# Optimization experiments

Measured on AMD Instinct MI355X. Metric: run time of the kernel, lower is better.

The kernel has to match this reference:

```python
import jax, jax.numpy as jnp
import numpy as np

B, S, DIM, H = 8, 1024, 768, 12
HD = DIM // H  # head_dim = 64
SCALE = HD ** -0.5


def setup_inputs() -> dict:
    key = jax.random.key(0)
    ks = jax.random.split(key, 9)
    std = DIM ** -0.5
    x = jax.random.normal(ks[0], (B, S, DIM), dtype=jnp.float32)
    Wq = jax.random.normal(ks[1], (DIM, DIM), dtype=jnp.float32) * std
    bq = jax.random.normal(ks[2], (DIM,), dtype=jnp.float32) * 0.01
    Wk = jax.random.normal(ks[3], (DIM, DIM), dtype=jnp.float32) * std
    bk = jax.random.normal(ks[4], (DIM,), dtype=jnp.float32) * 0.01
    Wv = jax.random.normal(ks[5], (DIM, DIM), dtype=jnp.float32) * std
    bv = jax.random.normal(ks[6], (DIM,), dtype=jnp.float32) * 0.01
    Wp = jax.random.normal(ks[7], (DIM, DIM), dtype=jnp.float32) * std
    bp = jax.random.normal(ks[8], (DIM,), dtype=jnp.float32) * 0.01
    return {"x": x, "Wq": Wq, "bq": bq, "Wk": Wk, "bk": bk,
            "Wv": Wv, "bv": bv, "Wp": Wp, "bp": bp}


def _split_heads(t):
    # [b, s, (n d)] -> [b, n, s, d]
    b, s, _ = t.shape
    return t.reshape(b, s, H, HD).transpose(0, 2, 1, 3)


def reference(x, Wq, bq, Wk, bk, Wv, bv, Wp, bp):
    q = _split_heads(x @ Wq + bq)
    k = _split_heads(x @ Wk + bk)
    v = _split_heads(x @ Wv + bv)
    attn = jnp.einsum('bnqd,bnkd->bnqk', q, k) * SCALE
    attn = jax.nn.softmax(attn, axis=-1)
    o = jnp.einsum('bnqk,bnkd->bnqd', attn, v)
    o = o.transpose(0, 2, 1, 3).reshape(x.shape[0], x.shape[1], DIM)
    return o @ Wp + bp
```

## Files before the change

### kernel.cpp

```cpp
#include <hip/hip_runtime.h>
#include <hip/hip_bf16.h>
#include <cstdint>

#define B_    8
#define S_    1024
#define DIM_  768
#define H_    12
#define HD_   64
#define QL2S_ 0.1803368801111204f

typedef __attribute__((ext_vector_type(8))) __bf16 bf16x8;
typedef __attribute__((ext_vector_type(4))) float  f32x4;

__device__ __forceinline__ short f2bf(float f) {
  union { float f; uint32_t u; } a;
  a.f = f;
  uint32_t u = a.u;
  uint32_t r = (u + 0x7FFFu + ((u >> 16) & 1u)) >> 16;
  return (short)r;
}

__device__ __forceinline__ float exp2a(float x) {
  float r;
  asm("v_exp_f32 %0, %1\n\ts_nop 1" : "=v"(r) : "v"(x));
  return r;
}

__device__ __forceinline__ void gll16(const void* g, void* l) {
  __builtin_amdgcn_global_load_lds((const __attribute__((address_space(1))) void*)g,
                                   (__attribute__((address_space(3))) void*)l, 16, 0, 0);
}

__device__ __forceinline__ int swz(int row, int col) {
  return row * 128 + ((((col >> 3) ^ (row & 7)) & 7) << 4) + ((col & 7) << 1);
}

__global__ __launch_bounds__(256) void k_cvt(const float* __restrict__ in,
                                             short* __restrict__ out, int n4) {
  int i = blockIdx.x * 256 + threadIdx.x;
  if (i >= n4) return;
  const float4 v = ((const float4*)in)[i];
  short4 o;
  o.x = f2bf(v.x); o.y = f2bf(v.y); o.z = f2bf(v.z); o.w = f2bf(v.w);
  ((short4*)out)[i] = o;
}

__global__ __launch_bounds__(256) void k_transpose4(const float* __restrict__ W0,
                                                    const float* __restrict__ W1,
                                                    const float* __restrict__ W2,
                                                    const float* __restrict__ W3,
                                                    short* o0, short* o1,
                                                    short* o2, short* o3) {
  const float* in = blockIdx.z == 0 ? W0 : blockIdx.z == 1 ? W1 : blockIdx.z == 2 ? W2 : W3;
  short* out = blockIdx.z == 0 ? o0 : blockIdx.z == 1 ? o1 : blockIdx.z == 2 ? o2 : o3;
  __shared__ float tile[32][33];
  const int tx = threadIdx.x, ty = threadIdx.y;
  const int bx = blockIdx.x * 32, by = blockIdx.y * 32;
#pragma unroll
  for (int j = 0; j < 32; j += 8)
    tile[ty + j][tx] = in[(size_t)(by + ty + j) * DIM_ + bx + tx];
  __syncthreads();
#pragma unroll
  for (int j = 0; j < 32; j += 8)
    out[(size_t)(bx + ty + j) * DIM_ + by + tx] = f2bf(tile[tx][ty + j]);
}

template <int MODE, bool QS>
__device__ __forceinline__ void gemm_body(char* smem,
                                          const short* __restrict__ A,
                                          const short* __restrict__ Bt,
                                          const float* __restrict__ bias,
                                          void* __restrict__ out,
                                          int bm, int bn) {
  char* As = smem;
  char* Bs = smem + 32768;
  const int tid = threadIdx.x;
  const int l = tid & 63, w = tid >> 6;
  const int hi = l >> 4, lo = l & 15;
  const int wr = w >> 1, wc = w & 1;

  auto stageA = [&](int ks, int bo) {
#pragma unroll
    for (int i = 0; i < 4; ++i) {
      const int gl = i * 256 + tid;
      const int row = gl >> 3;
      const int g = (gl & 7) ^ (row & 7);
      gll16(A + (size_t)(bm * 128 + row) * DIM_ + ks * 64 + g * 8, As + bo + gl * 16);
    }
  };
  auto stageB = [&](int ks, int bo) {
#pragma unroll
    for (int i = 0; i < 4; ++i) {
      const int gl = i * 256 + tid;
      const int row = gl >> 3;
      const int g = (gl & 7) ^ (row & 7);
      gll16(Bt + (size_t)(bn * 128 + row) * DIM_ + ks * 64 + g * 8, Bs + bo + gl * 16);
    }
  };

  f32x4 acc[4][4];
  const f32x4 zz = {0.f, 0.f, 0.f, 0.f};
#pragma unroll
  for (int m = 0; m < 4; ++m)
#pragma unroll
    for (int n = 0; n < 4; ++n) acc[m][n] = zz;

  stageA(0, 0);
  stageB(0, 0);
  __syncthreads();

  for (int ks = 0; ks < 12; ++ks) {
    const int cu = (ks & 1) << 14;
    if (ks < 11) { stageA(ks + 1, cu ^ 16384); stageB(ks + 1, cu ^ 16384); }
#pragma unroll
    for (int kk = 0; kk < 2; ++kk) {
      bf16x8 a[4], b[4];
#pragma unroll
      for (int m = 0; m < 4; ++m)
        a[m] = *(const bf16x8*)(As + cu + swz(wr * 64 + m * 16 + lo, kk * 32 + hi * 8));
#pragma unroll
      for (int n = 0; n < 4; ++n)
        b[n] = *(const bf16x8*)(Bs + cu + swz(wc * 64 + n * 16 + lo, kk * 32 + hi * 8));
#pragma unroll
      for (int m = 0; m < 4; ++m)
#pragma unroll
        for (int n = 0; n < 4; ++n)
          acc[m][n] = __builtin_amdgcn_mfma_f32_16x16x32_bf16(a[m], b[n], acc[m][n], 0, 0, 0);
    }
    __syncthreads();
  }

#pragma unroll
  for (int m = 0; m < 4; ++m) {
#pragma unroll
    for (int n = 0; n < 4; ++n) {
#pragma unroll
      for (int r = 0; r < 4; ++r) {
        const int R = bm * 128 + wr * 64 + m * 16 + hi * 4 + r;
        const int C = bn * 128 + wc * 64 + n * 16 + lo;
        float v = acc[m][n][r] + bias[MODE == 1 ? R : C];
        if (QS) v *= QL2S_;
        if (MODE == 0) {
          ((short*)out)[((size_t)((R >> 10) * H_ + (C >> 6)) * S_ + (R & 1023)) * HD_ + (C & 63)] = f2bf(v);
        } else if (MODE == 1) {
          ((short*)out)[((size_t)((C >> 10) * H_ + (R >> 6)) * HD_ + (R & 63)) * S_ + (C & 1023)] = f2bf(v);
        } else {
          ((float*)out)[(size_t)R * DIM_ + C] = v;
        }
      }
    }
  }
}

__global__ __launch_bounds__(256, 2) void k_gemm_qkv(const short* __restrict__ xb,
                                                     const short* __restrict__ WqT,
                                                     const short* __restrict__ WkT,
                                                     const short* __restrict__ WvT,
                                                     const float* __restrict__ bq,
                                                     const float* __restrict__ bk,
                                                     const float* __restrict__ bv,
                                                     short* qo, short* ko, short* vo) {
  __shared__ alignas(16) char smem[65536];
  if (blockIdx.z == 0)
    gemm_body<0, true>(smem, xb, WqT, bq, qo, blockIdx.x, blockIdx.y);
  else if (blockIdx.z == 1)
    gemm_body<0, false>(smem, xb, WkT, bk, ko, blockIdx.x, blockIdx.y);
  else
    gemm_body<1, false>(smem, WvT, xb, bv, vo, blockIdx.y, blockIdx.x);
}

__global__ __launch_bounds__(256, 2) void k_gemm_proj(const short* __restrict__ A,
                                                      const short* __restrict__ Bt,
                                                      const float* __restrict__ bias,
                                                      float* out) {
  __shared__ alignas(16) char smem[65536];
  gemm_body<2, false>(smem, A, Bt, bias, out, blockIdx.y, blockIdx.x);
}

__global__ __launch_bounds__(256, 3) void k_attn(const short* __restrict__ qw,
                                                 const short* __restrict__ kw,
                                                 const short* __restrict__ vtw,
                                                 short* __restrict__ ow) {
  __shared__ alignas(16) char smem[49152];
  char* Kb = smem;
  char* Vb = smem + 16384;
  char* Ps = smem + 32768;
  const int tid = threadIdx.x;
  const int l = tid & 63, w = tid >> 6;
  const int hi = l >> 4, lo = l & 15;
  const int qt = blockIdx.x & 7;
  const int bh = blockIdx.x >> 3;

  const short* qg = qw  + (size_t)bh * (S_ * HD_) + (qt * 128) * HD_;
  const short* kg = kw  + (size_t)bh * (S_ * HD_);
  const short* vg = vtw + (size_t)bh * (S_ * HD_);

  auto stage = [&](int T, int bufo) {
#pragma unroll
    for (int i = 0; i < 2; ++i) {
      const int gl = i * 256 + tid;
      const int row = gl >> 3;
      const int g = (gl & 7) ^ (row & 7);
      gll16(kg + (T * 64 + row) * 64 + g * 8, Kb + bufo + gl * 16);
    }
#pragma unroll
    for (int i = 0; i < 2; ++i) {
      const int gl = i * 256 + tid;
      const int row = gl >> 3;
      const int g = (gl & 7) ^ (row & 7);
      gll16(vg + row * 1024 + T * 64 + g * 8, Vb + bufo + gl * 16);
    }
  };

  bf16x8 aQ[2][2];
#pragma unroll
  for (int m = 0; m < 2; ++m)
#pragma unroll
    for (int kk = 0; kk < 2; ++kk)
      aQ[m][kk] = *(const bf16x8*)(qg + (w * 32 + m * 16 + lo) * HD_ + kk * 32 + hi * 8);

  f32x4 o_acc[2][4];
  const f32x4 zz = {0.f, 0.f, 0.f, 0.f};
#pragma unroll
  for (int m = 0; m < 2; ++m)
#pragma unroll
    for (int db = 0; db < 4; ++db) o_acc[m][db] = zz;
  float lsum[2][4];
#pragma unroll
  for (int m = 0; m < 2; ++m)
#pragma unroll
    for (int r = 0; r < 4; ++r) lsum[m][r] = 0.f;

  stage(0, 0);
  __syncthreads();

  for (int t = 0; t < 16; ++t) {
    const int cu = (t & 1) << 13;
    if (t < 15) stage(t + 1, cu ^ 8192);

    f32x4 sacc[2][4];
#pragma unroll
    for (int m = 0; m < 2; ++m)
#pragma unroll
      for (int nb = 0; nb < 4; ++nb) sacc[m][nb] = zz;
#pragma unroll
    for (int kk = 0; kk < 2; ++kk) {
#pragma unroll
      for (int nb = 0; nb < 4; ++nb) {
        const bf16x8 bK = *(const bf16x8*)(Kb + cu + swz(nb * 16 + lo, kk * 32 + hi * 8));
#pragma unroll
        for (int m = 0; m < 2; ++m)
          sacc[m][nb] = __builtin_amdgcn_mfma_f32_16x16x32_bf16(aQ[m][kk], bK, sacc[m][nb], 0, 0, 0);
      }
    }

#pragma unroll
    for (int m = 0; m < 2; ++m)
#pragma unroll
      for (int r = 0; r < 4; ++r)
#pragma unroll
        for (int nb = 0; nb < 4; ++nb) {
          const float p = exp2a(sacc[m][nb][r] - 1.0f);
          lsum[m][r] += p;
          *(short*)(Ps + swz(w * 32 + m * 16 + hi * 4 + r, nb * 16 + lo)) = f2bf(p);
        }
    asm volatile("s_waitcnt lgkmcnt(0)" ::: "memory");
    __builtin_amdgcn_sched_barrier(0);

#pragma unroll
    for (int kk = 0; kk < 2; ++kk) {
      bf16x8 aP[2];
#pragma unroll
      for (int m = 0; m < 2; ++m)
        aP[m] = *(const bf16x8*)(Ps + swz(w * 32 + m * 16 + lo, kk * 32 + hi * 8));
#pragma unroll
      for (int db = 0; db < 4; ++db) {
        const bf16x8 bV = *(const bf16x8*)(Vb + cu + swz(db * 16 + lo, kk * 32 + hi * 8));
#pragma unroll
        for (int m = 0; m < 2; ++m)
          o_acc[m][db] = __builtin_amdgcn_mfma_f32_16x16x32_bf16(aP[m], bV, o_acc[m][db], 0, 0, 0);
      }
    }

    __syncthreads();
  }

  const int b = bh / H_, h = bh % H_;
#pragma unroll
  for (int m = 0; m < 2; ++m) {
#pragma unroll
    for (int r = 0; r < 4; ++r) {
      float lr = lsum[m][r];
#pragma unroll
      for (int mask = 1; mask < 16; mask <<= 1) lr += __shfl_xor(lr, mask, 64);
      const float inv = 1.0f / lr;
      const int sg = qt * 128 + w * 32 + m * 16 + hi * 4 + r;
#pragma unroll
      for (int db = 0; db < 4; ++db)
        ow[((size_t)(b * S_ + sg)) * DIM_ + h * HD_ + db * 16 + lo] = f2bf(o_acc[m][db][r] * inv);
    }
  }
}

extern "C" void kernel_launch(void* const* d_in, const int* in_sizes, int n_in,
                              void* d_out, int out_size, void* d_ws, size_t ws_size,
                              hipStream_t stream) {
  const float* x  = (const float*)d_in[0];
  const float* Wq = (const float*)d_in[1];
  const float* bq = (const float*)d_in[2];
  const float* Wk = (const float*)d_in[3];
  const float* bk = (const float*)d_in[4];
  const float* Wv = (const float*)d_in[5];
  const float* bv = (const float*)d_in[6];
  const float* Wp = (const float*)d_in[7];
  const float* bp = (const float*)d_in[8];

  char* ws = (char*)d_ws;
  size_t off = 0;
  auto alloc = [&](size_t bytes) {
    char* p = ws + off;
    off += (bytes + 255) & ~(size_t)255;
    return p;
  };
  short* xb  = (short*)alloc((size_t)8192 * 768 * 2);
  short* WqT = (short*)alloc((size_t)768 * 768 * 2);
  short* WkT = (short*)alloc((size_t)768 * 768 * 2);
  short* WvT = (short*)alloc((size_t)768 * 768 * 2);
  short* WpT = (short*)alloc((size_t)768 * 768 * 2);
  short* qwv = (short*)alloc((size_t)96 * 1024 * 64 * 2);
  short* kwv = (short*)alloc((size_t)96 * 1024 * 64 * 2);
  short* vtw = (short*)alloc((size_t)96 * 1024 * 64 * 2);
  short* owv = (short*)alloc((size_t)8192 * 768 * 2);

  k_cvt<<<6144, 256, 0, stream>>>(x, xb, 8192 * 768 / 4);
  dim3 tb(32, 8), tg(24, 24, 4);
  k_transpose4<<<tg, tb, 0, stream>>>(Wq, Wk, Wv, Wp, WqT, WkT, WvT, WpT);

  k_gemm_qkv<<<dim3(64, 6, 3), 256, 0, stream>>>(xb, WqT, WkT, WvT, bq, bk, bv, qwv, kwv, vtw);

  k_attn<<<B_ * H_ * (S_ / 128), 256, 0, stream>>>(qwv, kwv, vtw, owv);

  k_gemm_proj<<<dim3(6, 64), 256, 0, stream>>>(owv, WpT, bp, (float*)d_out);
}
```

Before: 110.7 us.

## Transpose QK^T MFMA output so P stores pack into 8-byte writes

Swaps the MFMA operand order in the QK^T product, so each lane holds four consecutive key columns for a single query row instead of four rows. This lets the softmax probabilities be converted with packed v_cvt_pk_bf16_f32 and written to LDS as one 8-byte store per block, replacing four scalar short stores with software rounding. Row sums become one accumulator per m, reduced at the end with two cross-lane shuffles plus a lane broadcast instead of four-step shuffle trees. The packed conversion instruction may round differently from the previous manual rounding.

```diff
diff --git a/kernel.cpp b/kernel.cpp
--- a/kernel.cpp
+++ b/kernel.cpp
@@ -23,6 +23,12 @@
 __device__ __forceinline__ float exp2a(float x) {
   float r;
   asm("v_exp_f32 %0, %1\n\ts_nop 1" : "=v"(r) : "v"(x));
+  return r;
+}
+
+__device__ __forceinline__ uint32_t cvtpk(float a, float b) {
+  uint32_t r;
+  asm("v_cvt_pk_bf16_f32 %0, %1, %2" : "=v"(r) : "v"(a), "v"(b));
   return r;
 }
 
@@ -225,11 +231,7 @@
   for (int m = 0; m < 2; ++m)
 #pragma unroll
     for (int db = 0; db < 4; ++db) o_acc[m][db] = zz;
-  float lsum[2][4];
-#pragma unroll
-  for (int m = 0; m < 2; ++m)
-#pragma unroll
-    for (int r = 0; r < 4; ++r) lsum[m][r] = 0.f;
+  float lsum[2] = {0.f, 0.f};
 
   stage(0, 0);
   __syncthreads();
@@ -250,20 +252,25 @@
         const bf16x8 bK = *(const bf16x8*)(Kb + cu + swz(nb * 16 + lo, kk * 32 + hi * 8));
 #pragma unroll
         for (int m = 0; m < 2; ++m)
-          sacc[m][nb] = __builtin_amdgcn_mfma_f32_16x16x32_bf16(aQ[m][kk], bK, sacc[m][nb], 0, 0, 0);
+          sacc[m][nb] = __builtin_amdgcn_mfma_f32_16x16x32_bf16(bK, aQ[m][kk], sacc[m][nb], 0, 0, 0);
       }
     }
 
 #pragma unroll
-    for (int m = 0; m < 2; ++m)
-#pragma unroll
-      for (int r = 0; r < 4; ++r)
-#pragma unroll
-        for (int nb = 0; nb < 4; ++nb) {
-          const float p = exp2a(sacc[m][nb][r] - 1.0f);
-          lsum[m][r] += p;
-          *(short*)(Ps + swz(w * 32 + m * 16 + hi * 4 + r, nb * 16 + lo)) = f2bf(p);
-        }
+    for (int m = 0; m < 2; ++m) {
+#pragma unroll
+      for (int nb = 0; nb < 4; ++nb) {
+        const float p0 = exp2a(sacc[m][nb][0] - 1.0f);
+        const float p1 = exp2a(sacc[m][nb][1] - 1.0f);
+        const float p2 = exp2a(sacc[m][nb][2] - 1.0f);
+        const float p3 = exp2a(sacc[m][nb][3] - 1.0f);
+        lsum[m] += (p0 + p1) + (p2 + p3);
+        uint2 pk;
+        pk.x = cvtpk(p0, p1);
+        pk.y = cvtpk(p2, p3);
+        *(uint2*)(Ps + swz(w * 32 + m * 16 + lo, nb * 16 + hi * 4)) = pk;
+      }
+    }
     asm volatile("s_waitcnt lgkmcnt(0)" ::: "memory");
     __builtin_amdgcn_sched_barrier(0);
 
@@ -285,14 +292,20 @@
     __syncthreads();
   }
 
+  float lF[2];
+#pragma unroll
+  for (int m = 0; m < 2; ++m) {
+    float s = lsum[m];
+    s += __shfl_xor(s, 16, 64);
+    s += __shfl_xor(s, 32, 64);
+    lF[m] = s;
+  }
   const int b = bh / H_, h = bh % H_;
 #pragma unroll
   for (int m = 0; m < 2; ++m) {
 #pragma unroll
     for (int r = 0; r < 4; ++r) {
-      float lr = lsum[m][r];
-#pragma unroll
-      for (int mask = 1; mask < 16; mask <<= 1) lr += __shfl_xor(lr, mask, 64);
+      const float lr = __shfl(lF[m], hi * 4 + r, 64);
       const float inv = 1.0f / lr;
       const int sg = qt * 128 + w * 32 + m * 16 + hi * 4 + r;
 #pragma unroll
```

New measurement: 104.8 us. -5.3%, faster.
